# Kernel optimization log

Hardware: AMD Instinct MI355X
Metric: run time of the kernel (lower is better)

## Reference

```python
import jax, jax.numpy as jnp
import numpy as np

N = 100000   # nodes
E = 1600000  # edges
IN = 128
HEADS = 4
D = 128 // HEADS  # per-head hidden (DGL: hid_feats/num_heads = 32)
OUT = 64
NEG_SLOPE = 0.2


def gat_conv(h, src, dst, W, al, ar, b, apply_relu):
    """DGL-style GATConv. h:[N,F_in], W:[F_in,H*D], al/ar:[H,D], b:[H*D]."""
    Hn, Dd = al.shape
    ft = (h @ W).reshape(-1, Hn, Dd)                      # [N,H,D]
    el = jnp.sum(ft * al, axis=-1)                        # [N,H]
    er = jnp.sum(ft * ar, axis=-1)                        # [N,H]
    e = jax.nn.leaky_relu(el[src] + er[dst], NEG_SLOPE)   # [E,H]
    # edge softmax over incoming edges of each dst node (numerically stable)
    emax = jax.ops.segment_max(e, dst, num_segments=N)    # [N,H]
    ex = jnp.exp(e - emax[dst])                           # [E,H]
    denom = jax.ops.segment_sum(ex, dst, num_segments=N)  # [N,H]
    alpha = ex / denom[dst]                               # [E,H]
    msg = ft[src] * alpha[:, :, None]                     # [E,H,D]
    out = jax.ops.segment_sum(msg, dst, num_segments=N)   # [N,H,D]
    out = out + b.reshape(Hn, Dd)
    if apply_relu:
        out = jax.nn.relu(out)
    return out.reshape(-1, Hn * Dd)                       # flatten(1)


def setup_inputs() -> dict:
    key = jax.random.key(0)
    ks = jax.random.split(key, 16)
    features = jax.random.normal(ks[0], (N, IN), dtype=jnp.float32)
    src = jax.random.randint(ks[1], (E,), 0, N, dtype=jnp.int32)
    # guarantee every node has at least one in-edge (allow_zero_in_degree=False)
    dst = jnp.concatenate([jnp.arange(N, dtype=jnp.int32),
                           jax.random.randint(ks[2], (E - N,), 0, N, dtype=jnp.int32)])
    s = 0.05
    return {
        "features": features, "src": src, "dst": dst,
        "W0": jax.random.normal(ks[3], (IN, HEADS * D)) * s,
        "al0": jax.random.normal(ks[4], (HEADS, D)) * s,
        "ar0": jax.random.normal(ks[5], (HEADS, D)) * s,
        "b0": jnp.zeros((HEADS * D,), jnp.float32),
        "W1": jax.random.normal(ks[6], (HEADS * D, HEADS * D)) * s,
        "al1": jax.random.normal(ks[7], (HEADS, D)) * s,
        "ar1": jax.random.normal(ks[8], (HEADS, D)) * s,
        "b1": jnp.zeros((HEADS * D,), jnp.float32),
        "W2": jax.random.normal(ks[9], (HEADS * D, OUT)) * s,
        "al2": jax.random.normal(ks[10], (1, OUT)) * s,
        "ar2": jax.random.normal(ks[11], (1, OUT)) * s,
        "b2": jnp.zeros((OUT,), jnp.float32),
    }


def reference(features, src, dst, W0, al0, ar0, b0, W1, al1, ar1, b1, W2, al2, ar2, b2):
    # dropout is identity at inference time
    h = gat_conv(features, src, dst, W0, al0, ar0, b0, apply_relu=True)
    h = gat_conv(h, src, dst, W1, al1, ar1, b1, apply_relu=True)
    h = gat_conv(h, src, dst, W2, al2, ar2, b2, apply_relu=False)  # last layer: 1 head, no activation
    return h  # [N, OUT]
```

## Files before the change

### kernel.cpp

```cpp
#include <hip/hip_runtime.h>
#include <hip/hip_bf16.h>
#include <hip/hip_fp16.h>
#include <math.h>


constexpr int BSH = 9;
constexpr int EPB = 4096;

typedef __attribute__((ext_vector_type(8))) short bf16x8;
typedef __attribute__((ext_vector_type(4))) float f32x4;

__device__ __forceinline__ ushort bf16_rne(float f) {
    unsigned u = __float_as_uint(f);
    u += 0x7FFF + ((u >> 16) & 1);
    return (ushort)(u >> 16);
}
__device__ __forceinline__ float bf16_tof(ushort h) {
    return __uint_as_float(((unsigned)h) << 16);
}


__global__ __launch_bounds__(256) void ehist(const int* __restrict__ dst,
                                             int* __restrict__ cmat,
                                             int E, int nebs) {
    __shared__ int lh[256];
    const int t = threadIdx.x;
    lh[t] = 0;
    __syncthreads();
    const int base = blockIdx.x * EPB;
    const int cntE = min(EPB, E - base);
    for (int i = t; i < cntE; i += 256) atomicAdd(&lh[dst[base + i] >> BSH], 1);
    __syncthreads();
    cmat[t * nebs + blockIdx.x] = lh[t];
}

__global__ __launch_bounds__(512) void bscan(int* __restrict__ cmat,
                                             int* __restrict__ rowtot, int nebs) {
    __shared__ int sh[512];
    const int b = blockIdx.x, t = threadIdx.x;
    int v = (t < nebs) ? cmat[b * nebs + t] : 0;
    sh[t] = v;
    __syncthreads();
    for (int off = 1; off < 512; off <<= 1) {
        int u = (t >= off) ? sh[t - off] : 0;
        __syncthreads();
        sh[t] += u;
        __syncthreads();
    }
    if (t < nebs) cmat[b * nebs + t] = sh[t] - v;
    if (t == 511) rowtot[b] = sh[511];
}

__global__ __launch_bounds__(256) void bbase_scan(const int* __restrict__ rowtot,
                                                  int* __restrict__ bbase) {
    __shared__ int sh[256];
    const int t = threadIdx.x;
    int v = rowtot[t];
    sh[t] = v;
    __syncthreads();
    for (int off = 1; off < 256; off <<= 1) {
        int u = (t >= off) ? sh[t - off] : 0;
        __syncthreads();
        sh[t] += u;
        __syncthreads();
    }
    bbase[t] = sh[t] - v;
}

__global__ __launch_bounds__(256) void escatter(
    const int* __restrict__ src, const int* __restrict__ dst,
    const int* __restrict__ cmat, const int* __restrict__ bbase,
    unsigned long long* __restrict__ ebuf, int E, int nebs) {
    __shared__ unsigned long long sbuf[EPB];
    __shared__ int lh[256], lstart[256], lcur[256];
    const int t = threadIdx.x;
    const int base = blockIdx.x * EPB;
    const int cntE = min(EPB, E - base);

    lh[t] = 0;
    __syncthreads();
    for (int i = t; i < cntE; i += 256) atomicAdd(&lh[dst[base + i] >> BSH], 1);
    __syncthreads();
    {
        __shared__ int sh[256];
        int v = lh[t];
        sh[t] = v;
        __syncthreads();
        for (int off = 1; off < 256; off <<= 1) {
            int u = (t >= off) ? sh[t - off] : 0;
            __syncthreads();
            sh[t] += u;
            __syncthreads();
        }
        lstart[t] = sh[t] - v;
        lcur[t] = sh[t] - v;
    }
    __syncthreads();
    for (int i = t; i < cntE; i += 256) {
        int d = dst[base + i], s = src[base + i];
        int r = atomicAdd(&lcur[d >> BSH], 1);
        sbuf[r] = ((unsigned long long)d << 32) | (unsigned int)s;
    }
    __syncthreads();
    for (int j = t; j < cntE; j += 256) {
        unsigned long long v = sbuf[j];
        int bk = (int)(v >> 32) >> BSH;
        int gpos = bbase[bk] + cmat[bk * nebs + blockIdx.x] + (j - lstart[bk]);
        ebuf[gpos] = v;
    }
}

__global__ __launch_bounds__(512) void bucket_fill(
    const unsigned long long* __restrict__ ebuf, const int* __restrict__ bbase,
    int* __restrict__ rowptr, int* __restrict__ colx, int N, int E, int nbuck) {
    __shared__ int cnt[512], nxtl[512], sh[512];
    const int b = blockIdx.x, t = threadIdx.x;
    const int nodebase = b << BSH;
    const int nn = min(512, N - nodebase);
    const int estart = bbase[b];
    const int eend = (b + 1 < 256) ? bbase[b + 1] : E;

    cnt[t] = 0;
    __syncthreads();
    for (int i = estart + t; i < eend; i += 512)
        atomicAdd(&cnt[(int)(ebuf[i] >> 32) - nodebase], 1);
    __syncthreads();
    int v = cnt[t];
    sh[t] = v;
    __syncthreads();
    for (int off = 1; off < 512; off <<= 1) {
        int u = (t >= off) ? sh[t - off] : 0;
        __syncthreads();
        sh[t] += u;
        __syncthreads();
    }
    if (t < nn) rowptr[nodebase + t + 1] = estart + sh[t];
    if (b == 0 && t == 0) rowptr[0] = 0;
    nxtl[t] = estart + sh[t] - v;
    __syncthreads();
    for (int i = estart + t; i < eend; i += 512) {
        unsigned long long v2 = ebuf[i];
        int d = (int)(v2 >> 32) - nodebase;
        int pos = atomicAdd(&nxtl[d], 1);
        colx[pos] = (int)(unsigned int)v2;
    }
}


template <int FOUT>
__global__ __launch_bounds__(256) void wprep(const float* __restrict__ W,
                                             ushort* __restrict__ wsw) {
    constexpr int NT = FOUT / 16;
    int idx = blockIdx.x * 256 + threadIdx.x;
    if (idx >= 128 * FOUT / 4) return;
    float4 v = ((const float4*)W)[idx];
    int e0 = idx * 4;
    int k = e0 / FOUT, c0 = e0 - k * FOUT;
    int kstep = k >> 5, g = (k >> 3) & 3, i = k & 7;
    float vv[4] = {v.x, v.y, v.z, v.w};
#pragma unroll
    for (int d = 0; d < 4; ++d) {
        int c = c0 + d;
        int tile = c >> 4, l16 = c & 15;
        int lane = g * 16 + l16;
        ushort hi = bf16_rne(vv[d]);
        ushort lo = bf16_rne(vv[d] - bf16_tof(hi));
        size_t base = ((((size_t)kstep * NT + tile) * 2 + 0) * 64 + lane) * 8 + i;
        wsw[base] = hi;
        wsw[base + 512] = lo;
    }
}


template <int FOUT, int H, bool HOUT>
__global__ __launch_bounds__(256) void gemm_mfma(
    const float* __restrict__ hin, const ushort* __restrict__ wsw,
    const float* __restrict__ al, const float* __restrict__ ar,
    void* __restrict__ ftout, float* __restrict__ el, float* __restrict__ er,
    int nnodes) {
    constexpr int NT = FOUT / 16;
    constexpr int WHALF = 2 * NT * 2 * 64 * 8;
    __shared__ ushort Asw[4 * 4 * 2 * 64 * 8];
    __shared__ ushort Wsw[WHALF];

    const int tid = threadIdx.x;
    const int wv = tid >> 6, lane = tid & 63;
    const int nb = blockIdx.x * 64;

    {
        const int nloc = tid >> 2;
        const int qb = tid & 3;
        const int gw = nloc >> 4, m = nloc & 15;
        const int n = nb + nloc;
        const bool v = n < nnodes;
        const float4* hrow = (const float4*)&hin[(size_t)(v ? n : 0) * 128];
#pragma unroll
        for (int it = 0; it < 8; ++it) {
            int q = qb + it * 4;
            int k0 = q * 4;
            float4 x = v ? hrow[q] : make_float4(0.f, 0.f, 0.f, 0.f);
            int kstep = k0 >> 5, g = (k0 >> 3) & 3, i0 = k0 & 7;
            int laneA = g * 16 + m;
            size_t base =
                ((((size_t)gw * 4 + kstep) * 2 + 0) * 64 + laneA) * 8 + i0;
            float xs[4] = {x.x, x.y, x.z, x.w};
            ushort4 uh, ul;
            ushort h;
            h = bf16_rne(xs[0]); uh.x = h; ul.x = bf16_rne(xs[0] - bf16_tof(h));
            h = bf16_rne(xs[1]); uh.y = h; ul.y = bf16_rne(xs[1] - bf16_tof(h));
            h = bf16_rne(xs[2]); uh.z = h; ul.z = bf16_rne(xs[2] - bf16_tof(h));
            h = bf16_rne(xs[3]); uh.w = h; ul.w = bf16_rne(xs[3] - bf16_tof(h));
            *(ushort4*)&Asw[base] = uh;
            *(ushort4*)&Asw[base + 512] = ul;
        }
    }

    f32x4 acc[NT];
#pragma unroll
    for (int t = 0; t < NT; ++t) acc[t] = (f32x4){0.f, 0.f, 0.f, 0.f};

#pragma unroll
    for (int kh = 0; kh < 2; ++kh) {
        __syncthreads();
        {
            const uint4* srcp = (const uint4*)(wsw + (size_t)kh * WHALF);
            uint4* dstp = (uint4*)Wsw;
            constexpr int CNT = WHALF / 8;
#pragma unroll
            for (int ii = 0; ii < CNT / 256; ++ii)
                dstp[tid + ii * 256] = srcp[tid + ii * 256];
        }
        __syncthreads();

#pragma unroll
        for (int ks2 = 0; ks2 < 2; ++ks2) {
            const int kstep = kh * 2 + ks2;
            bf16x8 ahi = *(const bf16x8*)
                &Asw[(((wv * 4 + kstep) * 2 + 0) * 64 + lane) * 8];
            bf16x8 alo = *(const bf16x8*)
                &Asw[(((wv * 4 + kstep) * 2 + 1) * 64 + lane) * 8];
#pragma unroll
            for (int t = 0; t < NT; ++t) {
                bf16x8 bhi = *(const bf16x8*)
                    &Wsw[(((ks2 * NT + t) * 2 + 0) * 64 + lane) * 8];
                bf16x8 blo = *(const bf16x8*)
                    &Wsw[(((ks2 * NT + t) * 2 + 1) * 64 + lane) * 8];
                acc[t] = __builtin_amdgcn_mfma_f32_16x16x32_bf16(ahi, bhi, acc[t], 0, 0, 0);
                acc[t] = __builtin_amdgcn_mfma_f32_16x16x32_bf16(ahi, blo, acc[t], 0, 0, 0);
                acc[t] = __builtin_amdgcn_mfma_f32_16x16x32_bf16(alo, bhi, acc[t], 0, 0, 0);
            }
        }
    }

    const int g = lane >> 4, l16 = lane & 15;
    const int nrow0 = nb + wv * 16 + g * 4;

    if constexpr (H == 4) {
#pragma unroll
        for (int h = 0; h < 4; ++h) {
            float a0 = al[h * 32 + l16], a1 = al[h * 32 + 16 + l16];
            float r0 = ar[h * 32 + l16], r1 = ar[h * 32 + 16 + l16];
#pragma unroll
            for (int j = 0; j < 4; ++j) {
                float pl = acc[2 * h][j] * a0 + acc[2 * h + 1][j] * a1;
                float pr = acc[2 * h][j] * r0 + acc[2 * h + 1][j] * r1;
#pragma unroll
                for (int msk = 1; msk < 16; msk <<= 1) {
                    pl += __shfl_xor(pl, msk);
                    pr += __shfl_xor(pr, msk);
                }
                int n = nrow0 + j;
                if (l16 == 0 && n < nnodes) {
                    el[(size_t)n * 4 + h] = pl;
                    er[(size_t)n * 4 + h] = pr;
                }
            }
        }
    } else {
#pragma unroll
        for (int j = 0; j < 4; ++j) {
            float pl = 0.f, pr = 0.f;
#pragma unroll
            for (int t = 0; t < NT; ++t) {
                pl = fmaf(acc[t][j], al[t * 16 + l16], pl);
                pr = fmaf(acc[t][j], ar[t * 16 + l16], pr);
            }
#pragma unroll
            for (int msk = 1; msk < 16; msk <<= 1) {
                pl += __shfl_xor(pl, msk);
                pr += __shfl_xor(pr, msk);
            }
            int n = nrow0 + j;
            if (l16 == 0 && n < nnodes) {
                el[n] = pl;
                er[n] = pr;
            }
        }
    }

#pragma unroll
    for (int j = 0; j < 4; ++j) {
        int n = nrow0 + j;
        if (n < nnodes) {
            if constexpr (HOUT) {
                __half* fth = (__half*)ftout;
#pragma unroll
                for (int t = 0; t < NT; ++t)
                    fth[(size_t)n * FOUT + t * 16 + l16] =
                        __float2half_rn(acc[t][j]);
            } else {
                float* ftf = (float*)ftout;
#pragma unroll
                for (int t = 0; t < NT; ++t)
                    ftf[(size_t)n * FOUT + t * 16 + l16] = acc[t][j];
            }
        }
    }
}


template <int F, int H, bool RELU, bool HIN>
__global__ __launch_bounds__(256) void gat_aggregate(
    const int* __restrict__ rowptr, const int* __restrict__ colx,
    const float* __restrict__ el, const float* __restrict__ er,
    const void* __restrict__ ftv, const float* __restrict__ bias,
    float* __restrict__ out, int nnodes) {
    constexpr int CPL = F / 16;
    const int tid = threadIdx.x, wv = tid >> 6, lane = tid & 63;
    const int grp = lane >> 4, sub = lane & 15;
    const int n = blockIdx.x * 16 + wv * 4 + grp;
    const bool valid = n < nnodes;
    const int nn = valid ? n : 0;

    const int start = rowptr[nn];
    const int end = valid ? rowptr[nn + 1] : start;
    int md = end - start;
    md = max(md, __shfl_xor(md, 16));
    md = max(md, __shfl_xor(md, 32));
    const int nit = (md + 7) / 8;

    const int head = (H == 4) ? (sub >> 2) : 0;
    const float er_s = (H == 4) ? er[(size_t)nn * 4 + head] : er[nn];

    float sA = 0.f, sB = 0.f;
    float acc[CPL];
#pragma unroll
    for (int c = 0; c < CPL; ++c) acc[c] = 0.f;

    int idxA[4], idxB[4];
    float xA[4], xB[4];
    uint4 hA[4], hB[4];
    float4 fA[4], fB[4];

    auto issue = [&](int (&idxX)[4], float (&xX)[4], uint4 (&hX)[4],
                     float4 (&fX)[4], int e0) {
#pragma unroll
        for (int i = 0; i < 4; ++i) {
            int ee = e0 + i;
            idxX[i] = (ee < end) ? colx[ee] : -1;
        }
#pragma unroll
        for (int i = 0; i < 4; ++i) {
            int sn = (idxX[i] < 0) ? 0 : idxX[i];
            if constexpr (HIN) {
                const __half* fth = (const __half*)ftv;
                hX[i] = *(const uint4*)&fth[(size_t)sn * F + sub * 8];
            } else {
                const float* ftf = (const float*)ftv;
                fX[i] = *(const float4*)&ftf[(size_t)sn * F + sub * 4];
            }
            xX[i] = (H == 4) ? el[(size_t)sn * 4 + head] : el[sn];
        }
    };
    auto compute = [&](int (&idxX)[4], float (&xX)[4], uint4 (&hX)[4],
                       float4 (&fX)[4], float& sX) {
#pragma unroll
        for (int i = 0; i < 4; ++i) {
            float x = xX[i] + er_s;
            x = fmaxf(x, 0.2f * x);
            float p = __expf(x);
            p = (idxX[i] >= 0) ? p : 0.f;
            sX += p;
            if constexpr (HIN) {
                const __half* hv = (const __half*)&hX[i];
#pragma unroll
                for (int c = 0; c < CPL; ++c)
                    acc[c] = fmaf(p, __half2float(hv[c]), acc[c]);
            } else {
                acc[0] = fmaf(p, fX[i].x, acc[0]);
                acc[1] = fmaf(p, fX[i].y, acc[1]);
                acc[2] = fmaf(p, fX[i].z, acc[2]);
                acc[3] = fmaf(p, fX[i].w, acc[3]);
            }
        }
    };

    int e0 = start;
    issue(idxA, xA, hA, fA, e0);
    for (int it = 0; it < nit; ++it) {
        issue(idxB, xB, hB, fB, e0 + 4);
        compute(idxA, xA, hA, fA, sA);
        issue(idxA, xA, hA, fA, e0 + 8);
        compute(idxB, xB, hB, fB, sB);
        e0 += 8;
    }

    if (!valid) return;
    float s = sA + sB;
    float inv = 1.0f / s;
    float o[CPL];
#pragma unroll
    for (int c = 0; c < CPL; ++c) {
        o[c] = acc[c] * inv + bias[sub * CPL + c];
        if (RELU) o[c] = fmaxf(o[c], 0.f);
    }
    if constexpr (CPL == 8) {
        *(float4*)&out[(size_t)n * F + sub * 8] =
            make_float4(o[0], o[1], o[2], o[3]);
        *(float4*)&out[(size_t)n * F + sub * 8 + 4] =
            make_float4(o[4], o[5], o[6], o[7]);
    } else {
        *(float4*)&out[(size_t)n * F + sub * 4] =
            make_float4(o[0], o[1], o[2], o[3]);
    }
}


static inline size_t alignup(size_t x) { return (x + 255) & ~(size_t)255; }

extern "C" void kernel_launch(void* const* d_in, const int* in_sizes, int n_in,
                              void* d_out, int out_size, void* d_ws, size_t ws_size,
                              hipStream_t stream) {
    const float* features = (const float*)d_in[0];
    const int* src = (const int*)d_in[1];
    const int* dst = (const int*)d_in[2];
    const float* W0 = (const float*)d_in[3];
    const float* al0 = (const float*)d_in[4];
    const float* ar0 = (const float*)d_in[5];
    const float* b0 = (const float*)d_in[6];
    const float* W1 = (const float*)d_in[7];
    const float* al1 = (const float*)d_in[8];
    const float* ar1 = (const float*)d_in[9];
    const float* b1 = (const float*)d_in[10];
    const float* W2 = (const float*)d_in[11];
    const float* al2 = (const float*)d_in[12];
    const float* ar2 = (const float*)d_in[13];
    const float* b2 = (const float*)d_in[14];
    float* out = (float*)d_out;

    const int N = in_sizes[0] / 128;
    const int E = in_sizes[1];
    const int nebs = (E + EPB - 1) / EPB;
    const int nbuck = (N + 511) >> BSH;

    char* w = (char*)d_ws;
    int* rowptr = (int*)w;     w += alignup((size_t)(N + 1) * 4);
    int* colx = (int*)w;       w += alignup((size_t)E * 4);
    float* ft32 = (float*)w;   w += alignup((size_t)N * 64 * 4);
    __half* ft16 = (__half*)w; w += alignup((size_t)N * 128 * 2);
    float* hbuf = (float*)w;   w += alignup((size_t)N * 128 * 4);
    float* el = (float*)w;     w += alignup((size_t)N * 4 * 4);
    float* er = (float*)w;     w += alignup((size_t)N * 4 * 4);
    unsigned long long* ebuf = (unsigned long long*)w;
    w += alignup((size_t)E * 8);
    int* cmat = (int*)w;       w += alignup((size_t)256 * nebs * 4);
    int* rowtot = (int*)w;     w += alignup(256 * 4);
    int* bbase = (int*)w;      w += alignup(256 * 4);
    ushort* wsw0 = (ushort*)w; w += alignup(128 * 128 * 2 * 2);
    ushort* wsw1 = (ushort*)w; w += alignup(128 * 128 * 2 * 2);
    ushort* wsw2 = (ushort*)w; w += alignup(128 * 64 * 2 * 2);

    hipMemsetAsync(rowtot, 0, 256 * 4, stream);
    ehist<<<nebs, 256, 0, stream>>>(dst, cmat, E, nebs);
    bscan<<<nbuck, 512, 0, stream>>>(cmat, rowtot, nebs);
    bbase_scan<<<1, 256, 0, stream>>>(rowtot, bbase);
    escatter<<<nebs, 256, 0, stream>>>(src, dst, cmat, bbase, ebuf, E, nebs);
    bucket_fill<<<nbuck, 512, 0, stream>>>(ebuf, bbase, rowptr, colx, N, E, nbuck);

    wprep<128><<<16, 256, 0, stream>>>(W0, wsw0);
    wprep<128><<<16, 256, 0, stream>>>(W1, wsw1);
    wprep<64><<<8, 256, 0, stream>>>(W2, wsw2);

    const int gG = (N + 63) / 64;
    const int gAgg = (N + 15) / 16;

    gemm_mfma<128, 4, true><<<gG, 256, 0, stream>>>(features, wsw0, al0, ar0, ft16, el, er, N);
    gat_aggregate<128, 4, true, true><<<gAgg, 256, 0, stream>>>(rowptr, colx, el, er, ft16, b0, hbuf, N);

    gemm_mfma<128, 4, true><<<gG, 256, 0, stream>>>(hbuf, wsw1, al1, ar1, ft16, el, er, N);
    gat_aggregate<128, 4, true, true><<<gAgg, 256, 0, stream>>>(rowptr, colx, el, er, ft16, b1, hbuf, N);

    gemm_mfma<64, 1, false><<<gG, 256, 0, stream>>>(hbuf, wsw2, al2, ar2, ft32, el, er, N);
    gat_aggregate<64, 1, false, false><<<gAgg, 256, 0, stream>>>(rowptr, colx, el, er, ft32, b2, out, N);
}
```

Before: 363.6 us.

## Store hidden activations in fp16, pack edge keys to 32 bits, merge weight prep

Intermediate layer outputs are written as fp16 instead of fp32, and the next GEMM reads fp16 input, which halves activation read/write traffic. Edge sort keys are packed into 32-bit words (local dst in the high bits, src in the low 17 bits), which halves ebuf traffic. The three weight-prep launches are merged into one, the rowtot memset is dropped, and the aggregate edge-loading logic is simplified with clamped indices. The costs are lower precision in the hidden activations and a packing scheme that assumes node ids fit in 17 bits.

```diff
diff --git a/kernel.cpp b/kernel.cpp
--- a/kernel.cpp
+++ b/kernel.cpp
@@ -52,10 +52,10 @@
 }
 
 __global__ __launch_bounds__(256) void bbase_scan(const int* __restrict__ rowtot,
-                                                  int* __restrict__ bbase) {
+                                                  int* __restrict__ bbase, int nbuck) {
     __shared__ int sh[256];
     const int t = threadIdx.x;
-    int v = rowtot[t];
+    int v = (t < nbuck) ? rowtot[t] : 0;
     sh[t] = v;
     __syncthreads();
     for (int off = 1; off < 256; off <<= 1) {
@@ -70,9 +70,10 @@
 __global__ __launch_bounds__(256) void escatter(
     const int* __restrict__ src, const int* __restrict__ dst,
     const int* __restrict__ cmat, const int* __restrict__ bbase,
-    unsigned long long* __restrict__ ebuf, int E, int nebs) {
-    __shared__ unsigned long long sbuf[EPB];
-    __shared__ int lh[256], lstart[256], lcur[256];
+    unsigned* __restrict__ ebuf, int E, int nebs) {
+    __shared__ unsigned sbuf[EPB];
+    __shared__ unsigned char sbk[EPB];
+    __shared__ int lh[256], lstart[256], lcur[256], sh[256];
     const int t = threadIdx.x;
     const int base = blockIdx.x * EPB;
     const int cntE = min(EPB, E - base);
@@ -82,7 +83,6 @@
     for (int i = t; i < cntE; i += 256) atomicAdd(&lh[dst[base + i] >> BSH], 1);
     __syncthreads();
     {
-        __shared__ int sh[256];
         int v = lh[t];
         sh[t] = v;
         __syncthreads();
@@ -98,20 +98,21 @@
     __syncthreads();
     for (int i = t; i < cntE; i += 256) {
         int d = dst[base + i], s = src[base + i];
-        int r = atomicAdd(&lcur[d >> BSH], 1);
-        sbuf[r] = ((unsigned long long)d << 32) | (unsigned int)s;
+        int bk = d >> BSH;
+        int r = atomicAdd(&lcur[bk], 1);
+        sbuf[r] = ((unsigned)(d & 511) << 17) | (unsigned)s;
+        sbk[r] = (unsigned char)bk;
     }
     __syncthreads();
     for (int j = t; j < cntE; j += 256) {
-        unsigned long long v = sbuf[j];
-        int bk = (int)(v >> 32) >> BSH;
+        int bk = sbk[j];
         int gpos = bbase[bk] + cmat[bk * nebs + blockIdx.x] + (j - lstart[bk]);
-        ebuf[gpos] = v;
+        ebuf[gpos] = sbuf[j];
     }
 }
 
 __global__ __launch_bounds__(512) void bucket_fill(
-    const unsigned long long* __restrict__ ebuf, const int* __restrict__ bbase,
+    const unsigned* __restrict__ ebuf, const int* __restrict__ bbase,
     int* __restrict__ rowptr, int* __restrict__ colx, int N, int E, int nbuck) {
     __shared__ int cnt[512], nxtl[512], sh[512];
     const int b = blockIdx.x, t = threadIdx.x;
@@ -123,7 +124,7 @@
     cnt[t] = 0;
     __syncthreads();
     for (int i = estart + t; i < eend; i += 512)
-        atomicAdd(&cnt[(int)(ebuf[i] >> 32) - nodebase], 1);
+        atomicAdd(&cnt[ebuf[i] >> 17], 1);
     __syncthreads();
     int v = cnt[t];
     sh[t] = v;
@@ -139,19 +140,27 @@
     nxtl[t] = estart + sh[t] - v;
     __syncthreads();
     for (int i = estart + t; i < eend; i += 512) {
-        unsigned long long v2 = ebuf[i];
-        int d = (int)(v2 >> 32) - nodebase;
-        int pos = atomicAdd(&nxtl[d], 1);
-        colx[pos] = (int)(unsigned int)v2;
-    }
-}
-
-
-template <int FOUT>
-__global__ __launch_bounds__(256) void wprep(const float* __restrict__ W,
-                                             ushort* __restrict__ wsw) {
-    constexpr int NT = FOUT / 16;
-    int idx = blockIdx.x * 256 + threadIdx.x;
+        unsigned v2 = ebuf[i];
+        int dl = v2 >> 17;
+        int pos = atomicAdd(&nxtl[dl], 1);
+        colx[pos] = (int)(v2 & 0x1FFFFu);
+    }
+}
+
+
+__global__ __launch_bounds__(256) void wprep_all(
+    const float* __restrict__ W0, const float* __restrict__ W1,
+    const float* __restrict__ W2, ushort* __restrict__ o0,
+    ushort* __restrict__ o1, ushort* __restrict__ o2) {
+    int b = blockIdx.x;
+    const float* W;
+    ushort* o;
+    int FOUT, bb;
+    if (b < 16) { W = W0; o = o0; FOUT = 128; bb = b; }
+    else if (b < 32) { W = W1; o = o1; FOUT = 128; bb = b - 16; }
+    else { W = W2; o = o2; FOUT = 64; bb = b - 32; }
+    const int NT = FOUT / 16;
+    int idx = bb * 256 + threadIdx.x;
     if (idx >= 128 * FOUT / 4) return;
     float4 v = ((const float4*)W)[idx];
     int e0 = idx * 4;
@@ -166,15 +175,15 @@
         ushort hi = bf16_rne(vv[d]);
         ushort lo = bf16_rne(vv[d] - bf16_tof(hi));
         size_t base = ((((size_t)kstep * NT + tile) * 2 + 0) * 64 + lane) * 8 + i;
-        wsw[base] = hi;
-        wsw[base + 512] = lo;
-    }
-}
-
-
-template <int FOUT, int H, bool HOUT>
+        o[base] = hi;
+        o[base + 512] = lo;
+    }
+}
+
+
+template <int FOUT, int H, bool HOUT, bool HIN16>
 __global__ __launch_bounds__(256) void gemm_mfma(
-    const float* __restrict__ hin, const ushort* __restrict__ wsw,
+    const void* __restrict__ hinv, const ushort* __restrict__ wsw,
     const float* __restrict__ al, const float* __restrict__ ar,
     void* __restrict__ ftout, float* __restrict__ el, float* __restrict__ er,
     int nnodes) {
@@ -193,25 +202,56 @@
         const int gw = nloc >> 4, m = nloc & 15;
         const int n = nb + nloc;
         const bool v = n < nnodes;
-        const float4* hrow = (const float4*)&hin[(size_t)(v ? n : 0) * 128];
-#pragma unroll
-        for (int it = 0; it < 8; ++it) {
-            int q = qb + it * 4;
-            int k0 = q * 4;
-            float4 x = v ? hrow[q] : make_float4(0.f, 0.f, 0.f, 0.f);
-            int kstep = k0 >> 5, g = (k0 >> 3) & 3, i0 = k0 & 7;
-            int laneA = g * 16 + m;
-            size_t base =
-                ((((size_t)gw * 4 + kstep) * 2 + 0) * 64 + laneA) * 8 + i0;
-            float xs[4] = {x.x, x.y, x.z, x.w};
-            ushort4 uh, ul;
-            ushort h;
-            h = bf16_rne(xs[0]); uh.x = h; ul.x = bf16_rne(xs[0] - bf16_tof(h));
-            h = bf16_rne(xs[1]); uh.y = h; ul.y = bf16_rne(xs[1] - bf16_tof(h));
-            h = bf16_rne(xs[2]); uh.z = h; ul.z = bf16_rne(xs[2] - bf16_tof(h));
-            h = bf16_rne(xs[3]); uh.w = h; ul.w = bf16_rne(xs[3] - bf16_tof(h));
-            *(ushort4*)&Asw[base] = uh;
-            *(ushort4*)&Asw[base + 512] = ul;
+        if constexpr (HIN16) {
+            const __half* hrow = (const __half*)hinv + (size_t)(v ? n : 0) * 128;
+#pragma unroll
+            for (int it = 0; it < 4; ++it) {
+                int k0 = (qb + it * 4) * 8;
+                uint4 x = v ? *(const uint4*)&hrow[k0]
+                            : make_uint4(0, 0, 0, 0);
+                const __half* hp = (const __half*)&x;
+                int kstep = k0 >> 5, g = (k0 >> 3) & 3;
+                int laneA = g * 16 + m;
+                size_t base =
+                    ((((size_t)gw * 4 + kstep) * 2 + 0) * 64 + laneA) * 8;
+                ushort4 uh0, uh1, ul0, ul1;
+                float f;
+                ushort h;
+                f = __half2float(hp[0]); h = bf16_rne(f); uh0.x = h; ul0.x = bf16_rne(f - bf16_tof(h));
+                f = __half2float(hp[1]); h = bf16_rne(f); uh0.y = h; ul0.y = bf16_rne(f - bf16_tof(h));
+                f = __half2float(hp[2]); h = bf16_rne(f); uh0.z = h; ul0.z = bf16_rne(f - bf16_tof(h));
+                f = __half2float(hp[3]); h = bf16_rne(f); uh0.w = h; ul0.w = bf16_rne(f - bf16_tof(h));
+                f = __half2float(hp[4]); h = bf16_rne(f); uh1.x = h; ul1.x = bf16_rne(f - bf16_tof(h));
+                f = __half2float(hp[5]); h = bf16_rne(f); uh1.y = h; ul1.y = bf16_rne(f - bf16_tof(h));
+                f = __half2float(hp[6]); h = bf16_rne(f); uh1.z = h; ul1.z = bf16_rne(f - bf16_tof(h));
+                f = __half2float(hp[7]); h = bf16_rne(f); uh1.w = h; ul1.w = bf16_rne(f - bf16_tof(h));
+                *(ushort4*)&Asw[base] = uh0;
+                *(ushort4*)&Asw[base + 4] = uh1;
+                *(ushort4*)&Asw[base + 512] = ul0;
+                *(ushort4*)&Asw[base + 516] = ul1;
+            }
+        } else {
+            const float4* hrow =
+                (const float4*)((const float*)hinv + (size_t)(v ? n : 0) * 128);
+#pragma unroll
+            for (int it = 0; it < 8; ++it) {
+                int q = qb + it * 4;
+                int k0 = q * 4;
+                float4 x = v ? hrow[q] : make_float4(0.f, 0.f, 0.f, 0.f);
+                int kstep = k0 >> 5, g = (k0 >> 3) & 3, i0 = k0 & 7;
+                int laneA = g * 16 + m;
+                size_t base =
+                    ((((size_t)gw * 4 + kstep) * 2 + 0) * 64 + laneA) * 8 + i0;
+                float xs[4] = {x.x, x.y, x.z, x.w};
+                ushort4 uh, ul;
+                ushort h;
+                h = bf16_rne(xs[0]); uh.x = h; ul.x = bf16_rne(xs[0] - bf16_tof(h));
+                h = bf16_rne(xs[1]); uh.y = h; ul.y = bf16_rne(xs[1] - bf16_tof(h));
+                h = bf16_rne(xs[2]); uh.z = h; ul.z = bf16_rne(xs[2] - bf16_tof(h));
+                h = bf16_rne(xs[3]); uh.w = h; ul.w = bf16_rne(xs[3] - bf16_tof(h));
+                *(ushort4*)&Asw[base] = uh;
+                *(ushort4*)&Asw[base + 512] = ul;
+            }
         }
     }
 
@@ -319,12 +359,12 @@
 }
 
 
-template <int F, int H, bool RELU, bool HIN>
+template <int F, int H, bool RELU, bool HIN, bool HOUT16>
 __global__ __launch_bounds__(256) void gat_aggregate(
     const int* __restrict__ rowptr, const int* __restrict__ colx,
     const float* __restrict__ el, const float* __restrict__ er,
     const void* __restrict__ ftv, const float* __restrict__ bias,
-    float* __restrict__ out, int nnodes) {
+    void* __restrict__ outv, int nnodes) {
     constexpr int CPL = F / 16;
     const int tid = threadIdx.x, wv = tid >> 6, lane = tid & 63;
     const int grp = lane >> 4, sub = lane & 15;
@@ -347,39 +387,42 @@
 #pragma unroll
     for (int c = 0; c < CPL; ++c) acc[c] = 0.f;
 
-    int idxA[4], idxB[4];
     float xA[4], xB[4];
     uint4 hA[4], hB[4];
-    float4 fA[4], fB[4];
-
-    auto issue = [&](int (&idxX)[4], float (&xX)[4], uint4 (&hX)[4],
-                     float4 (&fX)[4], int e0) {
+
+    auto issue = [&](float (&xX)[4], uint4 (&hX)[4], int e0) {
 #pragma unroll
         for (int i = 0; i < 4; ++i) {
             int ee = e0 + i;
-            idxX[i] = (ee < end) ? colx[ee] : -1;
-        }
-#pragma unroll
-        for (int i = 0; i < 4; ++i) {
-            int sn = (idxX[i] < 0) ? 0 : idxX[i];
+            int eec = max(min(ee, end - 1), 0);
+            int sn = colx[eec];
             if constexpr (HIN) {
                 const __half* fth = (const __half*)ftv;
-                hX[i] = *(const uint4*)&fth[(size_t)sn * F + sub * 8];
+                if constexpr (CPL == 8) {
+                    hX[i] = *(const uint4*)&fth[(size_t)sn * F + sub * 8];
+                } else {
+                    uint2 t2 = *(const uint2*)&fth[(size_t)sn * F + sub * 4];
+                    hX[i].x = t2.x;
+                    hX[i].y = t2.y;
+                }
             } else {
                 const float* ftf = (const float*)ftv;
-                fX[i] = *(const float4*)&ftf[(size_t)sn * F + sub * 4];
+                float4 f = *(const float4*)&ftf[(size_t)sn * F + sub * 4];
+                hX[i].x = __float_as_uint(f.x);
+                hX[i].y = __float_as_uint(f.y);
+                hX[i].z = __float_as_uint(f.z);
+                hX[i].w = __float_as_uint(f.w);
             }
             xX[i] = (H == 4) ? el[(size_t)sn * 4 + head] : el[sn];
         }
     };
-    auto compute = [&](int (&idxX)[4], float (&xX)[4], uint4 (&hX)[4],
-                       float4 (&fX)[4], float& sX) {
+    auto compute = [&](float (&xX)[4], uint4 (&hX)[4], int e0, float& sX) {
 #pragma unroll
         for (int i = 0; i < 4; ++i) {
             float x = xX[i] + er_s;
             x = fmaxf(x, 0.2f * x);
             float p = __expf(x);
-            p = (idxX[i] >= 0) ? p : 0.f;
+            p = (e0 + i < end) ? p : 0.f;
             sX += p;
             if constexpr (HIN) {
                 const __half* hv = (const __half*)&hX[i];
@@ -387,21 +430,21 @@
                 for (int c = 0; c < CPL; ++c)
                     acc[c] = fmaf(p, __half2float(hv[c]), acc[c]);
             } else {
-                acc[0] = fmaf(p, fX[i].x, acc[0]);
-                acc[1] = fmaf(p, fX[i].y, acc[1]);
-                acc[2] = fmaf(p, fX[i].z, acc[2]);
-                acc[3] = fmaf(p, fX[i].w, acc[3]);
+                const float* fv = (const float*)&hX[i];
+#pragma unroll
+                for (int c = 0; c < CPL; ++c)
+                    acc[c] = fmaf(p, fv[c], acc[c]);
             }
         }
     };
 
     int e0 = start;
-    issue(idxA, xA, hA, fA, e0);
+    issue(xA, hA, e0);
     for (int it = 0; it < nit; ++it) {
-        issue(idxB, xB, hB, fB, e0 + 4);
-        compute(idxA, xA, hA, fA, sA);
-        issue(idxA, xA, hA, fA, e0 + 8);
-        compute(idxB, xB, hB, fB, sB);
+        issue(xB, hB, e0 + 4);
+        compute(xA, hA, e0, sA);
+        issue(xA, hA, e0 + 8);
+        compute(xB, hB, e0 + 4, sB);
         e0 += 8;
     }
 
@@ -414,14 +457,29 @@
         o[c] = acc[c] * inv + bias[sub * CPL + c];
         if (RELU) o[c] = fmaxf(o[c], 0.f);
     }
-    if constexpr (CPL == 8) {
-        *(float4*)&out[(size_t)n * F + sub * 8] =
-            make_float4(o[0], o[1], o[2], o[3]);
-        *(float4*)&out[(size_t)n * F + sub * 8 + 4] =
-            make_float4(o[4], o[5], o[6], o[7]);
+    if constexpr (HOUT16) {
+        __half* oh = (__half*)outv;
+        uint4 u;
+        ushort* up = (ushort*)&u;
+#pragma unroll
+        for (int c = 0; c < CPL; ++c)
+            up[c] = __half_as_ushort(__float2half_rn(o[c]));
+        if constexpr (CPL == 8) {
+            *(uint4*)&oh[(size_t)n * F + sub * 8] = u;
+        } else {
+            *(uint2*)&oh[(size_t)n * F + sub * 4] = make_uint2(u.x, u.y);
+        }
     } else {
-        *(float4*)&out[(size_t)n * F + sub * 4] =
-            make_float4(o[0], o[1], o[2], o[3]);
+        float* of = (float*)outv;
+        if constexpr (CPL == 8) {
+            *(float4*)&of[(size_t)n * F + sub * 8] =
+                make_float4(o[0], o[1], o[2], o[3]);
+            *(float4*)&of[(size_t)n * F + sub * 8 + 4] =
+                make_float4(o[4], o[5], o[6], o[7]);
+        } else {
+            *(float4*)&of[(size_t)n * F + sub * 4] =
+                make_float4(o[0], o[1], o[2], o[3]);
+        }
     }
 }
 
@@ -454,42 +512,38 @@
     const int nbuck = (N + 511) >> BSH;
 
     char* w = (char*)d_ws;
-    int* rowptr = (int*)w;     w += alignup((size_t)(N + 1) * 4);
-    int* colx = (int*)w;       w += alignup((size_t)E * 4);
-    float* ft32 = (float*)w;   w += alignup((size_t)N * 64 * 4);
-    __half* ft16 = (__half*)w; w += alignup((size_t)N * 128 * 2);
-    float* hbuf = (float*)w;   w += alignup((size_t)N * 128 * 4);
-    float* el = (float*)w;     w += alignup((size_t)N * 4 * 4);
-    float* er = (float*)w;     w += alignup((size_t)N * 4 * 4);
-    unsigned long long* ebuf = (unsigned long long*)w;
-    w += alignup((size_t)E * 8);
-    int* cmat = (int*)w;       w += alignup((size_t)256 * nebs * 4);
-    int* rowtot = (int*)w;     w += alignup(256 * 4);
-    int* bbase = (int*)w;      w += alignup(256 * 4);
-    ushort* wsw0 = (ushort*)w; w += alignup(128 * 128 * 2 * 2);
-    ushort* wsw1 = (ushort*)w; w += alignup(128 * 128 * 2 * 2);
-    ushort* wsw2 = (ushort*)w; w += alignup(128 * 64 * 2 * 2);
-
-    hipMemsetAsync(rowtot, 0, 256 * 4, stream);
+    int* rowptr = (int*)w;       w += alignup((size_t)(N + 1) * 4);
+    int* colx = (int*)w;         w += alignup((size_t)E * 4 + 256);
+    float* ft32 = (float*)w;     w += alignup((size_t)N * 64 * 4);
+    __half* ft16 = (__half*)w;   w += alignup((size_t)N * 128 * 2);
+    __half* hbuf16 = (__half*)w; w += alignup((size_t)N * 128 * 2);
+    float* el = (float*)w;       w += alignup((size_t)N * 4 * 4);
+    float* er = (float*)w;       w += alignup((size_t)N * 4 * 4);
+    unsigned* ebuf = (unsigned*)w; w += alignup((size_t)E * 4);
+    int* cmat = (int*)w;         w += alignup((size_t)256 * nebs * 4);
+    int* rowtot = (int*)w;       w += alignup(256 * 4);
+    int* bbase = (int*)w;        w += alignup(256 * 4);
+    ushort* wsw0 = (ushort*)w;   w += alignup(128 * 128 * 2 * 2);
+    ushort* wsw1 = (ushort*)w;   w += alignup(128 * 128 * 2 * 2);
+    ushort* wsw2 = (ushort*)w;   w += alignup(128 * 64 * 2 * 2);
+
     ehist<<<nebs, 256, 0, stream>>>(dst, cmat, E, nebs);
     bscan<<<nbuck, 512, 0, stream>>>(cmat, rowtot, nebs);
-    bbase_scan<<<1, 256, 0, stream>>>(rowtot, bbase);
+    bbase_scan<<<1, 256, 0, stream>>>(rowtot, bbase, nbuck);
     escatter<<<nebs, 256, 0, stream>>>(src, dst, cmat, bbase, ebuf, E, nebs);
     bucket_fill<<<nbuck, 512, 0, stream>>>(ebuf, bbase, rowptr, colx, N, E, nbuck);
 
-    wprep<128><<<16, 256, 0, stream>>>(W0, wsw0);
-    wprep<128><<<16, 256, 0, stream>>>(W1, wsw1);
-    wprep<64><<<8, 256, 0, stream>>>(W2, wsw2);
+    wprep_all<<<40, 256, 0, stream>>>(W0, W1, W2, wsw0, wsw1, wsw2);
 
     const int gG = (N + 63) / 64;
     const int gAgg = (N + 15) / 16;
 
-    gemm_mfma<128, 4, true><<<gG, 256, 0, stream>>>(features, wsw0, al0, ar0, ft16, el, er, N);
-    gat_aggregate<128, 4, true, true><<<gAgg, 256, 0, stream>>>(rowptr, colx, el, er, ft16, b0, hbuf, N);
-
-    gemm_mfma<128, 4, true><<<gG, 256, 0, stream>>>(hbuf, wsw1, al1, ar1, ft16, el, er, N);
-    gat_aggregate<128, 4, true, true><<<gAgg, 256, 0, stream>>>(rowptr, colx, el, er, ft16, b1, hbuf, N);
-
-    gemm_mfma<64, 1, false><<<gG, 256, 0, stream>>>(hbuf, wsw2, al2, ar2, ft32, el, er, N);
-    gat_aggregate<64, 1, false, false><<<gAgg, 256, 0, stream>>>(rowptr, colx, el, er, ft32, b2, out, N);
-}
+    gemm_mfma<128, 4, true, false><<<gG, 256, 0, stream>>>(features, wsw0, al0, ar0, ft16, el, er, N);
+    gat_aggregate<128, 4, true, true, true><<<gAgg, 256, 0, stream>>>(rowptr, colx, el, er, ft16, b0, hbuf16, N);
+
+    gemm_mfma<128, 4, true, true><<<gG, 256, 0, stream>>>(hbuf16, wsw1, al1, ar1, ft16, el, er, N);
+    gat_aggregate<128, 4, true, true, true><<<gAgg, 256, 0, stream>>>(rowptr, colx, el, er, ft16, b1, hbuf16, N);
+
+    gemm_mfma<64, 1, false, true><<<gG, 256, 0, stream>>>(hbuf16, wsw2, al2, ar2, ft32, el, er, N);
+    gat_aggregate<64, 1, false, false, false><<<gAgg, 256, 0, stream>>>(rowptr, colx, el, er, ft32, b2, out, N);
+}
```

Result: faster. 340.6 us (-6.3%).
